# Optimization experiments

Measured on AMD Instinct MI355X. Metric: run time of the kernel, lower is better.

The kernel has to match this reference:

```python
import jax, jax.numpy as jnp
import numpy as np

N_NODES = 20000
N_EDGES = 160000
N_GRAPHS = 64
VOCAB = 2 ** 16
EMBED_DIM = 32
IN_GNN = EMBED_DIM + 4  # 36
H1, H2 = 2048, 1024
N_CLASSES = 2  # task 'a'


def setup_inputs() -> dict:
    key = jax.random.key(0)
    ks = jax.random.split(key, 16)
    inp = {
        "node_type_ids": jax.random.randint(ks[0], (N_NODES,), 0, VOCAB, dtype=jnp.int32),
        "other_feats": jax.random.normal(ks[1], (N_NODES, 4), dtype=jnp.float32),
        "edge_index": jax.random.randint(ks[2], (2, N_EDGES), 0, N_NODES, dtype=jnp.int32),
        "batch": jnp.sort(jax.random.randint(ks[3], (N_NODES,), 0, N_GRAPHS, dtype=jnp.int32)),
        # parameters
        "emb": jax.random.normal(ks[4], (VOCAB, EMBED_DIM), dtype=jnp.float32),
        "W1": jax.random.normal(ks[5], (IN_GNN, H1), dtype=jnp.float32) * 0.05,
        "b1": jnp.zeros((H1,), jnp.float32),
        "W2": jax.random.normal(ks[6], (H1, H2), dtype=jnp.float32) * 0.02,
        "b2": jnp.zeros((H2,), jnp.float32),
        "hW1": jax.random.normal(ks[7], (H2, 1024), dtype=jnp.float32) * 0.02,
        "hb1": jnp.zeros((1024,), jnp.float32),
        "hW2": jax.random.normal(ks[8], (1024, 512), dtype=jnp.float32) * 0.02,
        "hb2": jnp.zeros((512,), jnp.float32),
        "oW": jax.random.normal(ks[9], (512, N_CLASSES), dtype=jnp.float32) * 0.02,
        "ob": jnp.zeros((N_CLASSES,), jnp.float32),
    }
    return inp


def _gcn_conv(x, W, b, src, dst, dinv):
    # PyG GCNConv (add_self_loops already applied in src/dst, dinv precomputed):
    # out_i = sum_{j->i} dinv[j]*dinv[i] * (x_j @ W) + b
    xw = x @ W  # [N, out]
    norm = dinv[src] * dinv[dst]  # [E']
    msg = xw[src] * norm[:, None]  # [E', out] -- dominant HBM traffic
    out = jax.ops.segment_sum(msg, dst, num_segments=x.shape[0])
    return out + b


def _forward(node_type_ids, other_feats, edge_index, batch,
             emb, W1, b1, W2, b2, hW1, hb1, hW2, hb2, oW, ob):
    n = other_feats.shape[0]
    # add self-loops (gcn_norm default)
    loop = jnp.arange(n, dtype=edge_index.dtype)
    src = jnp.concatenate([edge_index[0], loop])
    dst = jnp.concatenate([edge_index[1], loop])
    deg = jax.ops.segment_sum(jnp.ones(src.shape[0], other_feats.dtype), dst, num_segments=n)
    dinv = jnp.where(deg > 0, jax.lax.rsqrt(deg), 0.0)

    x = jnp.concatenate([emb[node_type_ids], other_feats], axis=-1)  # [N, 36]
    x = jax.nn.relu(_gcn_conv(x, W1, b1, src, dst, dinv))  # dropout is eval no-op
    x = jax.nn.relu(_gcn_conv(x, W2, b2, src, dst, dinv))

    # global mean pool over graphs
    counts = jax.ops.segment_sum(jnp.ones(n, x.dtype), batch, num_segments=N_GRAPHS)
    pooled = jax.ops.segment_sum(x, batch, num_segments=N_GRAPHS)
    pooled = pooled / jnp.maximum(counts, 1.0)[:, None]  # [G, 1024]

    h = jax.nn.relu(pooled @ hW1 + hb1)
    h = jax.nn.relu(h @ hW2 + hb2)
    return h @ oW + ob  # [G, 2]


def reference(node_type_ids, other_feats, edge_index, batch,
              emb, W1, b1, W2, b2, hW1, hb1, hW2, hb2, oW, ob):
    return _forward(node_type_ids, other_feats, edge_index, batch,
                    emb, W1, b1, W2, b2, hW1, hb1, hW2, hb2, oW, ob)
```

## Files before the change

### kernel.cpp

```cpp
#include <hip/hip_runtime.h>
#include <hip/hip_bf16.h>

#define N_NODES  20000
#define N_EDGES  160000
#define N_TOT_E  180000
#define N_GRAPHS 64
#define EMBED_DIM 32
#define IN_GNN   36
#define K1PAD    64
#define H1       2048
#define H2       1024
#define CHUNK0   10112

typedef unsigned short u16;
typedef short bf16x8 __attribute__((ext_vector_type(8)));
typedef float f32x4  __attribute__((ext_vector_type(4)));
typedef u16   u16x8  __attribute__((ext_vector_type(8)));

__device__ inline u16 f32_to_bf16(float f) {
    union { float f; unsigned u; } v; v.f = f;
    unsigned lsb = (v.u >> 16) & 1u;
    return (u16)((v.u + 0x7fffu + lsb) >> 16);
}
__device__ inline float bf16_to_f32(u16 h) {
    union { unsigned u; float f; } v; v.u = ((unsigned)h) << 16;
    return v.f;
}


__global__ void fill_i32(int* p, int v, int n) {
    int i = blockIdx.x * 256 + threadIdx.x;
    if (i < n) p[i] = v;
}

__global__ void deg_accum(const int* __restrict__ ei, int* indeg) {
    int e = blockIdx.x * 256 + threadIdx.x;
    if (e < N_EDGES) atomicAdd(&indeg[ei[N_EDGES + e]], 1);
}

__global__ void deg_to_dinv(const int* __restrict__ indeg, float* __restrict__ d) {
    int i = blockIdx.x * 256 + threadIdx.x;
    if (i < N_NODES) d[i] = rsqrtf((float)indeg[i]);
}

__global__ void build_xfeat(const int* __restrict__ ids, const float* __restrict__ other,
                            const float* __restrict__ emb, float* __restrict__ xf) {
    int idx = blockIdx.x * 256 + threadIdx.x;
    if (idx >= N_NODES * IN_GNN) return;
    int i = idx / IN_GNN;
    int d = idx - i * IN_GNN;
    float v = (d < EMBED_DIM) ? emb[(size_t)ids[i] * EMBED_DIM + d]
                              : other[i * 4 + (d - EMBED_DIM)];
    xf[idx] = v;
}

__global__ __launch_bounds__(1024) void scan_offsets(const int* __restrict__ indeg,
                                                     int* __restrict__ off,
                                                     int* __restrict__ cursor) {
    __shared__ int buf[1024];
    __shared__ int base_s;
    int tid = threadIdx.x;
    if (tid == 0) base_s = 0;
    __syncthreads();
    for (int start = 0; start < N_NODES; start += 1024) {
        int i = start + tid;
        int v = (i < N_NODES) ? indeg[i] : 0;
        buf[tid] = v;
        __syncthreads();
        for (int s = 1; s < 1024; s <<= 1) {
            int t = (tid >= s) ? buf[tid - s] : 0;
            __syncthreads();
            buf[tid] += t;
            __syncthreads();
        }
        int incl = buf[tid];
        int excl = incl - v;
        int base = base_s;
        if (i < N_NODES) {
            int o = base + excl;
            off[i] = o;
            cursor[i] = o;
        }
        __syncthreads();
        if (tid == 1023) base_s = base + incl;
        __syncthreads();
    }
    if (tid == 0) off[N_NODES] = N_TOT_E;
}

__global__ void csr_fill(const int* __restrict__ ei, const float* __restrict__ dinv,
                         int* __restrict__ cursor,
                         int* __restrict__ csr_src, float* __restrict__ csr_nrm) {
    int e = blockIdx.x * 256 + threadIdx.x;
    if (e >= N_TOT_E) return;
    int s, t;
    if (e < N_EDGES) { s = ei[e]; t = ei[N_EDGES + e]; }
    else             { s = t = e - N_EDGES; }
    int pos = atomicAdd(&cursor[t], 1);
    csr_src[pos] = s;
    csr_nrm[pos] = dinv[s] * dinv[t];
}

__global__ void agg_csr_36(const int* __restrict__ off, const int* __restrict__ csr_src,
                           const float* __restrict__ csr_nrm,
                           const float* __restrict__ xf,
                           u16* __restrict__ aggh, u16* __restrict__ aggl) {
    int idx = blockIdx.x * 256 + threadIdx.x;
    if (idx >= N_NODES * K1PAD) return;
    int node = idx >> 6;
    int d = idx & 63;
    u16 hi = 0, lo = 0;
    if (d < IN_GNN) {
        int p0 = off[node], p1 = off[node + 1];
        float acc = 0.0f;
        for (int p = p0; p < p1; p++)
            acc += xf[csr_src[p] * IN_GNN + d] * csr_nrm[p];
        hi = f32_to_bf16(acc);
        lo = f32_to_bf16(acc - bf16_to_f32(hi));
    }
    aggh[idx] = hi;
    aggl[idx] = lo;
}

__global__ void conv_w1(const float* __restrict__ W,
                        u16* __restrict__ Bh, u16* __restrict__ Bl) {
    int idx = blockIdx.x * 256 + threadIdx.x;
    if (idx >= H1 * K1PAD) return;
    int n = idx >> 6;
    int k = idx & 63;
    u16 hi = 0, lo = 0;
    if (k < IN_GNN) {
        float v = W[(size_t)k * H1 + n];
        hi = f32_to_bf16(v);
        lo = f32_to_bf16(v - bf16_to_f32(hi));
    }
    Bh[idx] = hi;
    Bl[idx] = lo;
}

__global__ __launch_bounds__(256) void conv_w2(const float* __restrict__ W,
                                               u16* __restrict__ Bh,
                                               u16* __restrict__ Bl) {
    __shared__ float t[32][33];
    int bk = blockIdx.x * 32;
    int bn = blockIdx.y * 32;
    int tx = threadIdx.x & 31, ty = threadIdx.x >> 5;
#pragma unroll
    for (int i = 0; i < 32; i += 8)
        t[ty + i][tx] = W[(size_t)(bk + ty + i) * H2 + bn + tx];
    __syncthreads();
#pragma unroll
    for (int i = 0; i < 32; i += 8) {
        float v = t[tx][ty + i];
        u16 hi = f32_to_bf16(v);
        u16 lo = f32_to_bf16(v - bf16_to_f32(hi));
        size_t o = (size_t)(bn + ty + i) * H1 + bk + tx;
        Bh[o] = hi;
        Bl[o] = lo;
    }
}

__global__ __launch_bounds__(256) void gemm1_mfma(const u16* __restrict__ Ah,
                                                  const u16* __restrict__ Al,
                                                  const u16* __restrict__ Bh,
                                                  const u16* __restrict__ Bl,
                                                  const float* __restrict__ bias,
                                                  u16* __restrict__ Xh,
                                                  u16* __restrict__ Xl,
                                                  int rowbase, int nrows) {
    __shared__ __align__(16) u16 lds[4][128 * K1PAD];
    const int tid  = threadIdx.x;
    const int wid  = tid >> 6;
    const int lane = tid & 63;
    const int wr   = wid >> 1, wc = wid & 1;
    const int row0 = blockIdx.y * 128;
    const int col0 = blockIdx.x * 128;

    const u16* gbase;
    int rbase; bool isA;
    if      (wid == 0) { gbase = Ah; rbase = row0; isA = true; }
    else if (wid == 1) { gbase = Al; rbase = row0; isA = true; }
    else if (wid == 2) { gbase = Bh; rbase = col0; isA = false; }
    else               { gbase = Bl; rbase = col0; isA = false; }
    u16* myl = lds[wid];
    const int r_l  = lane >> 3;
    const int ks_l = (lane & 7) * 8;
#pragma unroll
    for (int i = 0; i < 16; i++) {
        int r = rbase + i * 8 + r_l;
        if (isA) { int g = rowbase + ((r > nrows - 1) ? (nrows - 1) : r);
                   r = g; }
        const u16* g = gbase + (size_t)r * K1PAD + ks_l;
        __builtin_amdgcn_global_load_lds(
            (const __attribute__((address_space(1))) void*)g,
            (__attribute__((address_space(3))) void*)(myl + i * 512),
            16, 0, 0);
    }
    __syncthreads();

    f32x4 acc[4][4] = {};
#pragma unroll
    for (int ks = 0; ks < 2; ks++) {
        bf16x8 afh[4], afl[4];
#pragma unroll
        for (int mi = 0; mi < 4; mi++) {
            int r   = wr * 64 + mi * 16 + (lane & 15);
            int off = r * K1PAD + ks * 32 + (lane >> 4) * 8;
            afh[mi] = *(const bf16x8*)&lds[0][off];
            afl[mi] = *(const bf16x8*)&lds[1][off];
        }
#pragma unroll
        for (int ni = 0; ni < 4; ni++) {
            int c   = wc * 64 + ni * 16 + (lane & 15);
            int off = c * K1PAD + ks * 32 + (lane >> 4) * 8;
            bf16x8 bfh = *(const bf16x8*)&lds[2][off];
            bf16x8 bfl = *(const bf16x8*)&lds[3][off];
#pragma unroll
            for (int mi = 0; mi < 4; mi++) {
                acc[mi][ni] = __builtin_amdgcn_mfma_f32_16x16x32_bf16(afh[mi], bfh, acc[mi][ni], 0, 0, 0);
                acc[mi][ni] = __builtin_amdgcn_mfma_f32_16x16x32_bf16(afh[mi], bfl, acc[mi][ni], 0, 0, 0);
                acc[mi][ni] = __builtin_amdgcn_mfma_f32_16x16x32_bf16(afl[mi], bfh, acc[mi][ni], 0, 0, 0);
            }
        }
    }

    __syncthreads();
    float (*ldsF)[128] = (float (*)[128])(&lds[0][0]);
#pragma unroll
    for (int ni = 0; ni < 4; ni++) {
        int colL = wc * 64 + ni * 16 + (lane & 15);
        float bb = bias[col0 + colL];
#pragma unroll
        for (int mi = 0; mi < 4; mi++) {
#pragma unroll
            for (int j = 0; j < 4; j++) {
                int rowL = wr * 64 + mi * 16 + (lane >> 4) * 4 + j;
                ldsF[rowL][colL] = fmaxf(acc[mi][ni][j] + bb, 0.0f);
            }
        }
    }
    __syncthreads();
    int rL = tid >> 1;
    int cb = (tid & 1) * 8;
    int lr = row0 + rL;
    if (lr < nrows) {
        size_t gb = (size_t)lr * H1 + col0;
#pragma unroll
        for (int c = 0; c < 8; c++) {
            int col = c * 16 + cb;
            u16x8 hv, lv;
#pragma unroll
            for (int e = 0; e < 8; e++) {
                float v = ldsF[rL][col + e];
                u16 h = f32_to_bf16(v);
                hv[e] = h;
                lv[e] = f32_to_bf16(v - bf16_to_f32(h));
            }
            *(u16x8*)&Xh[gb + col] = hv;
            *(u16x8*)&Xl[gb + col] = lv;
        }
    }
}

__global__ __launch_bounds__(256) void gemm2_mfma(const u16* __restrict__ Ah,
                                                  const u16* __restrict__ Al,
                                                  const u16* __restrict__ Bh,
                                                  const u16* __restrict__ Bl,
                                                  float* __restrict__ C,
                                                  int rowbase, int nrows) {
    __shared__ u16 lds[4][128 * 32];
    const int tid  = threadIdx.x;
    const int wid  = tid >> 6;
    const int lane = tid & 63;
    const int wr   = wid >> 1, wc = wid & 1;

    int NB = (int)(gridDim.x * gridDim.y);
    int b  = (int)(blockIdx.y * gridDim.x + blockIdx.x);
    int lin = b;
    if ((NB & 7) == 0) {
        int xcd = b & 7, j = b >> 3;
        lin = xcd * (NB >> 3) + j;
    }
    const int col0 = (lin & 7) * 128;
    const int row0 = (lin >> 3) * 128;

    const u16* gbase;
    int rbase;
    if      (wid == 0) { gbase = Ah; rbase = row0; }
    else if (wid == 1) { gbase = Al; rbase = row0; }
    else if (wid == 2) { gbase = Bh; rbase = col0; }
    else               { gbase = Bl; rbase = col0; }
    u16* myl = lds[wid];
    const int r_l  = lane >> 2;
    const int ks_l = (lane & 3) * 8;

    int rows[8];
#pragma unroll
    for (int i = 0; i < 8; i++) {
        int r = rbase + i * 16 + r_l;
        if (wid < 2 && r > nrows - 1) r = nrows - 1;
        rows[i] = r;
    }

    f32x4 acc[4][4] = {};

    for (int kt = 0; kt < H1 / 32; ++kt) {
        int k0 = kt * 32;
        __syncthreads();
#pragma unroll
        for (int i = 0; i < 8; i++) {
            const u16* g = gbase + (size_t)rows[i] * H1 + k0 + ks_l;
            __builtin_amdgcn_global_load_lds(
                (const __attribute__((address_space(1))) void*)g,
                (__attribute__((address_space(3))) void*)(myl + i * 512),
                16, 0, 0);
        }
        __syncthreads();

        bf16x8 afh[4], afl[4];
#pragma unroll
        for (int mi = 0; mi < 4; mi++) {
            int r   = wr * 64 + mi * 16 + (lane & 15);
            int off = r * 32 + (lane >> 4) * 8;
            afh[mi] = *(const bf16x8*)&lds[0][off];
            afl[mi] = *(const bf16x8*)&lds[1][off];
        }
#pragma unroll
        for (int ni = 0; ni < 4; ni++) {
            int c   = wc * 64 + ni * 16 + (lane & 15);
            int off = c * 32 + (lane >> 4) * 8;
            bf16x8 bfh = *(const bf16x8*)&lds[2][off];
            bf16x8 bfl = *(const bf16x8*)&lds[3][off];
#pragma unroll
            for (int mi = 0; mi < 4; mi++) {
                acc[mi][ni] = __builtin_amdgcn_mfma_f32_16x16x32_bf16(afh[mi], bfh, acc[mi][ni], 0, 0, 0);
                acc[mi][ni] = __builtin_amdgcn_mfma_f32_16x16x32_bf16(afh[mi], bfl, acc[mi][ni], 0, 0, 0);
                acc[mi][ni] = __builtin_amdgcn_mfma_f32_16x16x32_bf16(afl[mi], bfh, acc[mi][ni], 0, 0, 0);
            }
        }
    }

#pragma unroll
    for (int mi = 0; mi < 4; mi++) {
#pragma unroll
        for (int ni = 0; ni < 4; ni++) {
            int col = col0 + wc * 64 + ni * 16 + (lane & 15);
#pragma unroll
            for (int j = 0; j < 4; j++) {
                int lr = row0 + wr * 64 + mi * 16 + (lane >> 4) * 4 + j;
                if (lr < nrows) C[(size_t)(rowbase + lr) * H2 + col] = acc[mi][ni][j];
            }
        }
    }
}

__global__ __launch_bounds__(256) void agg_csr_1024(const int* __restrict__ off,
                                                    const int* __restrict__ csr_src,
                                                    const float* __restrict__ csr_nrm,
                                                    const float* __restrict__ xw,
                                                    const float* __restrict__ b,
                                                    float* __restrict__ x2) {
    int node = blockIdx.x;
    int p0 = off[node], p1 = off[node + 1];
    int d = threadIdx.x;
    float4 a0 = make_float4(0.f, 0.f, 0.f, 0.f);
    float4 a1 = make_float4(0.f, 0.f, 0.f, 0.f);
    int p = p0;
    for (; p + 1 < p1; p += 2) {
        int   s0 = csr_src[p],     s1 = csr_src[p + 1];
        float n0 = csr_nrm[p],     n1 = csr_nrm[p + 1];
        float4 v0 = ((const float4*)&xw[(size_t)s0 * H2])[d];
        float4 v1 = ((const float4*)&xw[(size_t)s1 * H2])[d];
        a0.x += v0.x * n0; a0.y += v0.y * n0; a0.z += v0.z * n0; a0.w += v0.w * n0;
        a1.x += v1.x * n1; a1.y += v1.y * n1; a1.z += v1.z * n1; a1.w += v1.w * n1;
    }
    if (p < p1) {
        int   s0 = csr_src[p];
        float n0 = csr_nrm[p];
        float4 v0 = ((const float4*)&xw[(size_t)s0 * H2])[d];
        a0.x += v0.x * n0; a0.y += v0.y * n0; a0.z += v0.z * n0; a0.w += v0.w * n0;
    }
    float4 bb = ((const float4*)b)[d];
    float4 o;
    o.x = fmaxf(a0.x + a1.x + bb.x, 0.f);
    o.y = fmaxf(a0.y + a1.y + bb.y, 0.f);
    o.z = fmaxf(a0.z + a1.z + bb.z, 0.f);
    o.w = fmaxf(a0.w + a1.w + bb.w, 0.f);
    ((float4*)&x2[(size_t)node * H2])[d] = o;
}

__global__ void cnt_accum(const int* __restrict__ batch, float* cnt) {
    int i = blockIdx.x * 256 + threadIdx.x;
    if (i < N_NODES) atomicAdd(&cnt[batch[i]], 1.0f);
}

__global__ void pool_accum(const int* __restrict__ batch, const float* __restrict__ x2,
                           float* __restrict__ pooled) {
    int d  = blockIdx.x * 256 + threadIdx.x;
    int i0 = blockIdx.y * 64;
    float acc = 0.0f;
    int gprev = -1;
    for (int i = 0; i < 64; i++) {
        int node = i0 + i;
        if (node >= N_NODES) break;
        int g = batch[node];
        if (g != gprev) {
            if (gprev >= 0) atomicAdd(&pooled[gprev * H2 + d], acc);
            acc = 0.0f; gprev = g;
        }
        acc += x2[(size_t)node * H2 + d];
    }
    if (gprev >= 0) atomicAdd(&pooled[gprev * H2 + d], acc);
}

__global__ void pool_norm(float* pooled, const float* cnt) {
    int idx = blockIdx.x * 256 + threadIdx.x;
    if (idx < N_GRAPHS * H2) {
        int g = idx >> 10;
        pooled[idx] /= fmaxf(cnt[g], 1.0f);
    }
}

__global__ __launch_bounds__(256) void head_gemm(const float* __restrict__ In,
                                                 const float* __restrict__ W,
                                                 float* __restrict__ Out, int K, int N) {
    __shared__ __align__(16) float As[16][256];
    int n  = blockIdx.x * 256 + threadIdx.x;
    int m0 = blockIdx.y * 16;
    int k0 = blockIdx.z * 256;
    for (int t = threadIdx.x; t < 16 * 256; t += 256) {
        int r = t >> 8, k = t & 255;
        As[r][k] = In[(size_t)(m0 + r) * K + k0 + k];
    }
    __syncthreads();
    float acc[16] = {};
    for (int k = 0; k < 256; k += 4) {
        float w0 = W[(size_t)(k0 + k + 0) * N + n];
        float w1 = W[(size_t)(k0 + k + 1) * N + n];
        float w2 = W[(size_t)(k0 + k + 2) * N + n];
        float w3 = W[(size_t)(k0 + k + 3) * N + n];
#pragma unroll
        for (int r = 0; r < 16; r++) {
            float4 a = *(const float4*)&As[r][k];
            acc[r] += a.x * w0 + a.y * w1 + a.z * w2 + a.w * w3;
        }
    }
    for (int r = 0; r < 16; r++)
        atomicAdd(&Out[(size_t)(m0 + r) * N + n], acc[r]);
}

__global__ void bias_relu_MN(float* __restrict__ x, const float* __restrict__ b,
                             int N, int total) {
    int idx = blockIdx.x * 256 + threadIdx.x;
    if (idx < total) {
        int d = idx & (N - 1);
        x[idx] = fmaxf(x[idx] + b[d], 0.0f);
    }
}

__global__ void head3(const float* __restrict__ h2, const float* __restrict__ oW,
                      const float* __restrict__ ob, float* __restrict__ out) {
    int tid = threadIdx.x;
    if (tid >= 128) return;
    int m = tid >> 1, c = tid & 1;
    float acc = 0.0f;
    for (int k = 0; k < 512; k++) acc += h2[m * 512 + k] * oW[k * 2 + c];
    out[tid] = acc + ob[c];
}

extern "C" void kernel_launch(void* const* d_in, const int* in_sizes, int n_in,
                              void* d_out, int out_size, void* d_ws, size_t ws_size,
                              hipStream_t stream) {
    const int*   ids   = (const int*)d_in[0];
    const float* other = (const float*)d_in[1];
    const int*   ei    = (const int*)d_in[2];
    const int*   batch = (const int*)d_in[3];
    const float* emb   = (const float*)d_in[4];
    const float* W1    = (const float*)d_in[5];
    const float* b1    = (const float*)d_in[6];
    const float* W2    = (const float*)d_in[7];
    const float* b2    = (const float*)d_in[8];
    const float* hW1   = (const float*)d_in[9];
    const float* hb1   = (const float*)d_in[10];
    const float* hW2   = (const float*)d_in[11];
    const float* hb2   = (const float*)d_in[12];
    const float* oW    = (const float*)d_in[13];
    const float* ob    = (const float*)d_in[14];
    float* out = (float*)d_out;

    char* ws = (char*)d_ws;
    size_t off_b = 0;
    auto alloc = [&](size_t bytes) {
        size_t p = (off_b + 255) & ~(size_t)255;
        off_b = p + bytes;
        return p;
    };
    size_t o_dinv = alloc((size_t)N_NODES * 4);
    size_t o_indeg= alloc((size_t)(N_NODES + 1) * 4);
    size_t o_off  = alloc((size_t)(N_NODES + 1) * 4);
    size_t o_cur  = alloc((size_t)N_NODES * 4);
    size_t o_csrc = alloc((size_t)N_TOT_E * 4);
    size_t o_cnrm = alloc((size_t)N_TOT_E * 4);
    size_t o_xf   = alloc((size_t)N_NODES * IN_GNN * 4);
    size_t o_aggh = alloc((size_t)N_NODES * K1PAD * 2);
    size_t o_aggl = alloc((size_t)N_NODES * K1PAD * 2);
    size_t o_w1h  = alloc((size_t)H1 * K1PAD * 2);
    size_t o_w1l  = alloc((size_t)H1 * K1PAD * 2);
    size_t o_x1h  = alloc((size_t)CHUNK0 * H1 * 2);
    size_t o_x1l  = alloc((size_t)CHUNK0 * H1 * 2);
    size_t o_w2h  = alloc((size_t)H2 * H1 * 2);
    size_t o_w2l  = alloc((size_t)H2 * H1 * 2);
    size_t o_xw2  = alloc((size_t)N_NODES * H2 * 4);
    size_t o_pool = alloc((size_t)N_GRAPHS * H2 * 4);
    size_t o_cnt  = alloc((size_t)N_GRAPHS * 4);
    size_t o_h1   = alloc((size_t)N_GRAPHS * 1024 * 4);
    size_t o_h2   = alloc((size_t)N_GRAPHS * 512 * 4);

    float* dinv = (float*)(ws + o_dinv);
    int*   indeg= (int*)(ws + o_indeg);
    int*   offs = (int*)(ws + o_off);
    int*   cur  = (int*)(ws + o_cur);
    int*   csrc = (int*)(ws + o_csrc);
    float* cnrm = (float*)(ws + o_cnrm);
    float* xf   = (float*)(ws + o_xf);
    u16*   aggh = (u16*)(ws + o_aggh);
    u16*   aggl = (u16*)(ws + o_aggl);
    u16*   w1h  = (u16*)(ws + o_w1h);
    u16*   w1l  = (u16*)(ws + o_w1l);
    u16*   x1h  = (u16*)(ws + o_x1h);
    u16*   x1l  = (u16*)(ws + o_x1l);
    u16*   w2h  = (u16*)(ws + o_w2h);
    u16*   w2l  = (u16*)(ws + o_w2l);
    float* xw2  = (float*)(ws + o_xw2);
    float* x2   = (float*)(ws + o_x1h);
    float* pooled = (float*)(ws + o_pool);
    float* cnt  = (float*)(ws + o_cnt);
    float* h1   = (float*)(ws + o_h1);
    float* h2   = (float*)(ws + o_h2);

    fill_i32<<<(N_NODES + 255) / 256, 256, 0, stream>>>(indeg, 1, N_NODES);
    deg_accum<<<(N_EDGES + 255) / 256, 256, 0, stream>>>(ei, indeg);
    deg_to_dinv<<<(N_NODES + 255) / 256, 256, 0, stream>>>(indeg, dinv);

    scan_offsets<<<1, 1024, 0, stream>>>(indeg, offs, cur);
    csr_fill<<<(N_TOT_E + 255) / 256, 256, 0, stream>>>(ei, dinv, cur, csrc, cnrm);

    build_xfeat<<<(N_NODES * IN_GNN + 255) / 256, 256, 0, stream>>>(ids, other, emb, xf);
    agg_csr_36<<<(N_NODES * K1PAD + 255) / 256, 256, 0, stream>>>(offs, csrc, cnrm, xf, aggh, aggl);

    conv_w1<<<(H1 * K1PAD + 255) / 256, 256, 0, stream>>>(W1, w1h, w1l);
    conv_w2<<<dim3(H1 / 32, H2 / 32), 256, 0, stream>>>(W2, w2h, w2l);

    {
        const int c0 = CHUNK0, c1 = N_NODES - CHUNK0;
        gemm1_mfma<<<dim3(H1 / 128, c0 / 128), 256, 0, stream>>>(aggh, aggl, w1h, w1l, b1, x1h, x1l, 0, c0);
        gemm2_mfma<<<dim3(H2 / 128, c0 / 128), 256, 0, stream>>>(x1h, x1l, w2h, w2l, xw2, 0, c0);
        gemm1_mfma<<<dim3(H1 / 128, (c1 + 127) / 128), 256, 0, stream>>>(aggh, aggl, w1h, w1l, b1, x1h, x1l, c0, c1);
        gemm2_mfma<<<dim3(H2 / 128, (c1 + 127) / 128), 256, 0, stream>>>(x1h, x1l, w2h, w2l, xw2, c0, c1);
    }

    agg_csr_1024<<<N_NODES, 256, 0, stream>>>(offs, csrc, cnrm, xw2, b2, x2);

    hipMemsetAsync(pooled, 0, (size_t)N_GRAPHS * H2 * 4, stream);
    hipMemsetAsync(cnt, 0, (size_t)N_GRAPHS * 4, stream);
    cnt_accum<<<(N_NODES + 255) / 256, 256, 0, stream>>>(batch, cnt);
    pool_accum<<<dim3(H2 / 256, (N_NODES + 63) / 64), 256, 0, stream>>>(batch, x2, pooled);
    pool_norm<<<(N_GRAPHS * H2 + 255) / 256, 256, 0, stream>>>(pooled, cnt);

    hipMemsetAsync(h1, 0, (size_t)N_GRAPHS * 1024 * 4, stream);
    head_gemm<<<dim3(1024 / 256, 4, 1024 / 256), 256, 0, stream>>>(pooled, hW1, h1, 1024, 1024);
    bias_relu_MN<<<(N_GRAPHS * 1024 + 255) / 256, 256, 0, stream>>>(h1, hb1, 1024, N_GRAPHS * 1024);

    hipMemsetAsync(h2, 0, (size_t)N_GRAPHS * 512 * 4, stream);
    head_gemm<<<dim3(512 / 256, 4, 1024 / 256), 256, 0, stream>>>(h1, hW2, h2, 1024, 512);
    bias_relu_MN<<<(N_GRAPHS * 512 + 255) / 256, 256, 0, stream>>>(h2, hb2, 512, N_GRAPHS * 512);

    head3<<<1, 128, 0, stream>>>(h2, oW, ob, out);
}
```

Baseline: 886.1 us.

## Store layer-1 activations as single fp16 and use 2-term fp16 MFMA in GEMM2

The hidden activation X1 is now stored as one fp16 array instead of a bf16 hi/lo pair. W2 is split into fp16 hi/lo, so GEMM2 issues two f16 MFMAs per tile instead of three bf16 ones. This halves X1 write/read traffic, cuts MFMA work by about a third, and lets both GEMMs run over all nodes in one launch each instead of two chunks. The trade is lower accuracy for X1: fp16 has an 11-bit mantissa and a limited range, so post-ReLU activations could lose precision or overflow.

```diff
diff --git a/kernel.cpp b/kernel.cpp
--- a/kernel.cpp
+++ b/kernel.cpp
@@ -10,12 +10,13 @@
 #define K1PAD    64
 #define H1       2048
 #define H2       1024
-#define CHUNK0   10112
+#define NPANELS  157
 
 typedef unsigned short u16;
 typedef short bf16x8 __attribute__((ext_vector_type(8)));
 typedef float f32x4  __attribute__((ext_vector_type(4)));
-typedef u16   u16x8  __attribute__((ext_vector_type(8)));
+typedef _Float16 f16;
+typedef f16  f16x8  __attribute__((ext_vector_type(8)));
 
 __device__ inline u16 f32_to_bf16(float f) {
     union { float f; unsigned u; } v; v.f = f;
@@ -26,6 +27,7 @@
     union { unsigned u; float f; } v; v.u = ((unsigned)h) << 16;
     return v.f;
 }
+__device__ inline u16 f16_bits(f16 h) { union { f16 h; u16 u; } v; v.h = h; return v.u; }
 
 
 __global__ void fill_i32(int* p, int v, int n) {
@@ -152,11 +154,11 @@
 #pragma unroll
     for (int i = 0; i < 32; i += 8) {
         float v = t[tx][ty + i];
-        u16 hi = f32_to_bf16(v);
-        u16 lo = f32_to_bf16(v - bf16_to_f32(hi));
+        f16 h = (f16)v;
+        f16 l = (f16)(v - (float)h);
         size_t o = (size_t)(bn + ty + i) * H1 + bk + tx;
-        Bh[o] = hi;
-        Bl[o] = lo;
+        Bh[o] = f16_bits(h);
+        Bl[o] = f16_bits(l);
     }
 }
 
@@ -165,9 +167,7 @@
                                                   const u16* __restrict__ Bh,
                                                   const u16* __restrict__ Bl,
                                                   const float* __restrict__ bias,
-                                                  u16* __restrict__ Xh,
-                                                  u16* __restrict__ Xl,
-                                                  int rowbase, int nrows) {
+                                                  u16* __restrict__ Xf) {
     __shared__ __align__(16) u16 lds[4][128 * K1PAD];
     const int tid  = threadIdx.x;
     const int wid  = tid >> 6;
@@ -188,8 +188,7 @@
 #pragma unroll
     for (int i = 0; i < 16; i++) {
         int r = rbase + i * 8 + r_l;
-        if (isA) { int g = rowbase + ((r > nrows - 1) ? (nrows - 1) : r);
-                   r = g; }
+        if (isA && r > N_NODES - 1) r = N_NODES - 1;
         const u16* g = gbase + (size_t)r * K1PAD + ks_l;
         __builtin_amdgcn_global_load_lds(
             (const __attribute__((address_space(1))) void*)g,
@@ -243,32 +242,25 @@
     int rL = tid >> 1;
     int cb = (tid & 1) * 8;
     int lr = row0 + rL;
-    if (lr < nrows) {
+    if (lr < N_NODES) {
         size_t gb = (size_t)lr * H1 + col0;
 #pragma unroll
         for (int c = 0; c < 8; c++) {
             int col = c * 16 + cb;
-            u16x8 hv, lv;
-#pragma unroll
-            for (int e = 0; e < 8; e++) {
-                float v = ldsF[rL][col + e];
-                u16 h = f32_to_bf16(v);
-                hv[e] = h;
-                lv[e] = f32_to_bf16(v - bf16_to_f32(h));
-            }
-            *(u16x8*)&Xh[gb + col] = hv;
-            *(u16x8*)&Xl[gb + col] = lv;
-        }
-    }
-}
-
-__global__ __launch_bounds__(256) void gemm2_mfma(const u16* __restrict__ Ah,
-                                                  const u16* __restrict__ Al,
+            u16 hv[8];
+#pragma unroll
+            for (int e = 0; e < 8; e++)
+                hv[e] = f16_bits((f16)ldsF[rL][col + e]);
+            *(f16x8*)&Xf[gb + col] = *(f16x8*)hv;
+        }
+    }
+}
+
+__global__ __launch_bounds__(256) void gemm2_mfma(const u16* __restrict__ Af,
                                                   const u16* __restrict__ Bh,
                                                   const u16* __restrict__ Bl,
-                                                  float* __restrict__ C,
-                                                  int rowbase, int nrows) {
-    __shared__ u16 lds[4][128 * 32];
+                                                  float* __restrict__ C) {
+    __shared__ u16 ldsA[128 * 32], ldsBh[128 * 32], ldsBl[128 * 32];
     const int tid  = threadIdx.x;
     const int wid  = tid >> 6;
     const int lane = tid & 63;
@@ -276,21 +268,17 @@
 
     int NB = (int)(gridDim.x * gridDim.y);
     int b  = (int)(blockIdx.y * gridDim.x + blockIdx.x);
-    int lin = b;
-    if ((NB & 7) == 0) {
-        int xcd = b & 7, j = b >> 3;
-        lin = xcd * (NB >> 3) + j;
-    }
+    int lin = (b & 7) * (NB >> 3) + (b >> 3);
     const int col0 = (lin & 7) * 128;
     const int row0 = (lin >> 3) * 128;
 
     const u16* gbase;
-    int rbase;
-    if      (wid == 0) { gbase = Ah; rbase = row0; }
-    else if (wid == 1) { gbase = Al; rbase = row0; }
-    else if (wid == 2) { gbase = Bh; rbase = col0; }
-    else               { gbase = Bl; rbase = col0; }
-    u16* myl = lds[wid];
+    u16* mybase;
+    int rbase, niter;
+    if      (wid == 0) { gbase = Af; mybase = ldsA;          rbase = row0;      niter = 4; }
+    else if (wid == 1) { gbase = Af; mybase = ldsA + 2048;   rbase = row0 + 64; niter = 4; }
+    else if (wid == 2) { gbase = Bh; mybase = ldsBh;         rbase = col0;      niter = 8; }
+    else               { gbase = Bl; mybase = ldsBl;         rbase = col0;      niter = 8; }
     const int r_l  = lane >> 2;
     const int ks_l = (lane & 3) * 8;
 
@@ -298,7 +286,7 @@
 #pragma unroll
     for (int i = 0; i < 8; i++) {
         int r = rbase + i * 16 + r_l;
-        if (wid < 2 && r > nrows - 1) r = nrows - 1;
+        if (wid < 2 && r > N_NODES - 1) r = N_NODES - 1;
         rows[i] = r;
     }
 
@@ -307,35 +295,32 @@
     for (int kt = 0; kt < H1 / 32; ++kt) {
         int k0 = kt * 32;
         __syncthreads();
-#pragma unroll
-        for (int i = 0; i < 8; i++) {
+        for (int i = 0; i < niter; i++) {
             const u16* g = gbase + (size_t)rows[i] * H1 + k0 + ks_l;
             __builtin_amdgcn_global_load_lds(
                 (const __attribute__((address_space(1))) void*)g,
-                (__attribute__((address_space(3))) void*)(myl + i * 512),
+                (__attribute__((address_space(3))) void*)(mybase + i * 512),
                 16, 0, 0);
         }
         __syncthreads();
 
-        bf16x8 afh[4], afl[4];
+        f16x8 af[4];
 #pragma unroll
         for (int mi = 0; mi < 4; mi++) {
             int r   = wr * 64 + mi * 16 + (lane & 15);
             int off = r * 32 + (lane >> 4) * 8;
-            afh[mi] = *(const bf16x8*)&lds[0][off];
-            afl[mi] = *(const bf16x8*)&lds[1][off];
+            af[mi] = *(const f16x8*)&ldsA[off];
         }
 #pragma unroll
         for (int ni = 0; ni < 4; ni++) {
             int c   = wc * 64 + ni * 16 + (lane & 15);
             int off = c * 32 + (lane >> 4) * 8;
-            bf16x8 bfh = *(const bf16x8*)&lds[2][off];
-            bf16x8 bfl = *(const bf16x8*)&lds[3][off];
+            f16x8 bfh = *(const f16x8*)&ldsBh[off];
+            f16x8 bfl = *(const f16x8*)&ldsBl[off];
 #pragma unroll
             for (int mi = 0; mi < 4; mi++) {
-                acc[mi][ni] = __builtin_amdgcn_mfma_f32_16x16x32_bf16(afh[mi], bfh, acc[mi][ni], 0, 0, 0);
-                acc[mi][ni] = __builtin_amdgcn_mfma_f32_16x16x32_bf16(afh[mi], bfl, acc[mi][ni], 0, 0, 0);
-                acc[mi][ni] = __builtin_amdgcn_mfma_f32_16x16x32_bf16(afl[mi], bfh, acc[mi][ni], 0, 0, 0);
+                acc[mi][ni] = __builtin_amdgcn_mfma_f32_16x16x32_f16(af[mi], bfh, acc[mi][ni], 0, 0, 0);
+                acc[mi][ni] = __builtin_amdgcn_mfma_f32_16x16x32_f16(af[mi], bfl, acc[mi][ni], 0, 0, 0);
             }
         }
     }
@@ -348,7 +333,7 @@
 #pragma unroll
             for (int j = 0; j < 4; j++) {
                 int lr = row0 + wr * 64 + mi * 16 + (lane >> 4) * 4 + j;
-                if (lr < nrows) C[(size_t)(rowbase + lr) * H2 + col] = acc[mi][ni][j];
+                if (lr < N_NODES) C[(size_t)lr * H2 + col] = acc[mi][ni][j];
             }
         }
     }
@@ -506,8 +491,7 @@
     size_t o_aggl = alloc((size_t)N_NODES * K1PAD * 2);
     size_t o_w1h  = alloc((size_t)H1 * K1PAD * 2);
     size_t o_w1l  = alloc((size_t)H1 * K1PAD * 2);
-    size_t o_x1h  = alloc((size_t)CHUNK0 * H1 * 2);
-    size_t o_x1l  = alloc((size_t)CHUNK0 * H1 * 2);
+    size_t o_x1f  = alloc((size_t)N_NODES * H1 * 2);
     size_t o_w2h  = alloc((size_t)H2 * H1 * 2);
     size_t o_w2l  = alloc((size_t)H2 * H1 * 2);
     size_t o_xw2  = alloc((size_t)N_NODES * H2 * 4);
@@ -527,12 +511,11 @@
     u16*   aggl = (u16*)(ws + o_aggl);
     u16*   w1h  = (u16*)(ws + o_w1h);
     u16*   w1l  = (u16*)(ws + o_w1l);
-    u16*   x1h  = (u16*)(ws + o_x1h);
-    u16*   x1l  = (u16*)(ws + o_x1l);
+    u16*   x1f  = (u16*)(ws + o_x1f);
     u16*   w2h  = (u16*)(ws + o_w2h);
     u16*   w2l  = (u16*)(ws + o_w2l);
     float* xw2  = (float*)(ws + o_xw2);
-    float* x2   = (float*)(ws + o_x1h);
+    float* x2   = (float*)(ws + o_x1f);
     float* pooled = (float*)(ws + o_pool);
     float* cnt  = (float*)(ws + o_cnt);
     float* h1   = (float*)(ws + o_h1);
@@ -551,13 +534,9 @@
     conv_w1<<<(H1 * K1PAD + 255) / 256, 256, 0, stream>>>(W1, w1h, w1l);
     conv_w2<<<dim3(H1 / 32, H2 / 32), 256, 0, stream>>>(W2, w2h, w2l);
 
-    {
-        const int c0 = CHUNK0, c1 = N_NODES - CHUNK0;
-        gemm1_mfma<<<dim3(H1 / 128, c0 / 128), 256, 0, stream>>>(aggh, aggl, w1h, w1l, b1, x1h, x1l, 0, c0);
-        gemm2_mfma<<<dim3(H2 / 128, c0 / 128), 256, 0, stream>>>(x1h, x1l, w2h, w2l, xw2, 0, c0);
-        gemm1_mfma<<<dim3(H1 / 128, (c1 + 127) / 128), 256, 0, stream>>>(aggh, aggl, w1h, w1l, b1, x1h, x1l, c0, c1);
-        gemm2_mfma<<<dim3(H2 / 128, (c1 + 127) / 128), 256, 0, stream>>>(x1h, x1l, w2h, w2l, xw2, c0, c1);
-    }
+    gemm1_mfma<<<dim3(H1 / 128, NPANELS), 256, 0, stream>>>(aggh, aggl, w1h, w1l, b1, x1f);
+
+    gemm2_mfma<<<dim3(H2 / 128, NPANELS), 256, 0, stream>>>(x1f, w2h, w2l, xw2);
 
     agg_csr_1024<<<N_NODES, 256, 0, stream>>>(offs, csrc, cnrm, xw2, b2, x2);
 
```

Result: faster. 839.3 us (-5.3%).
